# Performance work log

Hardware: AMD Instinct MI355X
Metric: run time of the kernel (lower is better)

The kernel has to match this reference:

```python
import jax, jax.numpy as jnp
import numpy as np

B, N, E, A, H, NT, TE = 2, 20000, 20000, 8, 256, 16, 32


def layer_norm(x, g, b, eps=1e-5):
    mu = x.mean(-1, keepdims=True)
    var = ((x - mu) ** 2).mean(-1, keepdims=True)
    return (x - mu) * jax.lax.rsqrt(var + eps) * g + b


def setup_inputs() -> dict:
    key = jax.random.key(0)
    ks = jax.random.split(key, 12)
    node_features = jax.random.normal(ks[0], (B, N, H), jnp.float32)
    hyperedge_members = jax.random.randint(ks[1], (B, E, A), 0, N)
    hyperedge_types = jax.random.randint(ks[2], (B, E), 0, NT)
    hyperedge_mask = jax.random.bernoulli(ks[3], 0.8, (B, E, A))
    edge_type_table = jax.random.normal(ks[4], (NT, TE), jnp.float32)
    W_enc = jax.random.normal(ks[5], (H + TE, H), jnp.float32) / np.sqrt(H + TE)
    b_enc = jnp.zeros((H,), jnp.float32)
    g_enc = jnp.ones((H,), jnp.float32)
    be_enc = jnp.zeros((H,), jnp.float32)
    W_upd = jax.random.normal(ks[6], (2 * H, H), jnp.float32) / np.sqrt(2 * H)
    b_upd = jnp.zeros((H,), jnp.float32)
    g_upd = jnp.ones((H,), jnp.float32)
    be_upd = jnp.zeros((H,), jnp.float32)
    return dict(node_features=node_features, hyperedge_members=hyperedge_members,
                hyperedge_types=hyperedge_types, hyperedge_mask=hyperedge_mask,
                edge_type_table=edge_type_table, W_enc=W_enc, b_enc=b_enc,
                g_enc=g_enc, be_enc=be_enc, W_upd=W_upd, b_upd=b_upd,
                g_upd=g_upd, be_upd=be_upd)


def reference(node_features, hyperedge_members, hyperedge_types, hyperedge_mask,
              edge_type_table, W_enc, b_enc, g_enc, be_enc,
              W_upd, b_upd, g_upd, be_upd):
    b, n, h = node_features.shape
    members = jnp.clip(hyperedge_members, 0, n - 1)          # [B,E,A]
    m = hyperedge_mask.astype(node_features.dtype)           # [B,E,A]

    # gather member features per hyperedge: [B,E,A,H]
    gathered = jax.vmap(lambda nf, idx: nf[idx])(node_features, members)
    gathered = gathered * m[..., None]
    cnt = jnp.clip(m.sum(-1, keepdims=True), 1.0, None)       # [B,E,1]
    pooled = gathered.sum(2) / cnt                            # [B,E,H]

    edge_emb = edge_type_table[hyperedge_types]               # [B,E,32]
    x = jnp.concatenate([pooled, edge_emb], -1) @ W_enc + b_enc
    edge_feat = layer_norm(jax.nn.gelu(x, approximate=False), g_enc, be_enc)  # [B,E,H]

    # scatter-add edge features back to member nodes (masked)
    def scat(ef, idx, mm):
        contrib = (ef[:, None, :] * mm[..., None]).reshape(-1, h)   # [E*A,H]
        flat = idx.reshape(-1)
        upd = jnp.zeros((n, h), ef.dtype).at[flat].add(contrib)
        c = jnp.zeros((n,), ef.dtype).at[flat].add(mm.reshape(-1))
        return upd, c

    upd, c = jax.vmap(scat)(edge_feat, members, m)            # [B,N,H], [B,N]
    upd = upd / jnp.clip(c, 1.0, None)[..., None]

    y = jnp.concatenate([node_features, upd], -1) @ W_upd + b_upd
    return layer_norm(jax.nn.gelu(y, approximate=False), g_upd, be_upd)
```

## Files before the change

### kernel.cpp

```cpp
#include <hip/hip_runtime.h>
#include <math.h>

#define Bq 2
#define Nn 20000
#define Ee 20000
#define Aa 8
#define Hh 256
#define TEe 32
#define NTy 16
constexpr int BE   = Bq * Ee;
constexpr int BN   = Bq * Nn;
constexpr int KTE  = 8;
constexpr int KTU  = 16;
constexpr int LDA  = 264;
constexpr int CAP  = 64;
constexpr int PB_DET  = 256;
constexpr int PB_PKE  = 32;
constexpr int PB_PKU  = 64;
constexpr int PB_TB   = 1;
constexpr int PB_ZD   = 64;
constexpr int NPREP   = PB_DET + PB_PKE + PB_PKU + PB_TB + PB_ZD + 1;
constexpr int NFD     = 1875;
constexpr int NFILL3  = NFD / 3;

typedef __attribute__((ext_vector_type(8))) short bf16x8;
typedef __attribute__((ext_vector_type(8))) unsigned short u16x8;
typedef __attribute__((ext_vector_type(4))) float f32x4;
typedef unsigned short u16;
typedef unsigned int   u32;

__device__ __forceinline__ u16 f2bf(float f) {
    u32 u = __float_as_uint(f);
    u32 r = u + 0x7FFFu + ((u >> 16) & 1u);
    return (u16)(r >> 16);
}
__device__ __forceinline__ float bf2f(u16 h) {
    return __uint_as_float(((u32)h) << 16);
}
__device__ __forceinline__ float gelu_f(float x) {
    return 0.5f * x * (1.f + erff(x * 0.70710678118654752440f));
}
__device__ __forceinline__ f32x4 mfma16(bf16x8 a, bf16x8 b, f32x4 c) {
    return __builtin_amdgcn_mfma_f32_16x16x32_bf16(a, b, c, 0, 0, 0);
}

__device__ __forceinline__ float mask_at(const void* mp, int flag, int i) {
    if (flag & 2) return ((const float*)mp)[i];
    if (flag & 1) return ((const unsigned char*)mp)[i] ? 1.f : 0.f;
    return ((const int*)mp)[i] ? 1.f : 0.f;
}

__global__ __launch_bounds__(256) void k_prep(
    const unsigned int* __restrict__ mw, int nmw, int* __restrict__ flag,
    const float* __restrict__ Wenc, u16* __restrict__ WeP,
    const float* __restrict__ Wupd, u16* __restrict__ WuP,
    const float* __restrict__ ett, const float* __restrict__ benc,
    float* __restrict__ tb, int* __restrict__ deg,
    float4* __restrict__ dummy) {
    __shared__ float s_e[NTy * TEe];
    const int bid = blockIdx.x;
    const int tid = threadIdx.x;

    if (bid < PB_DET) {
        int found = 0;
        for (int i = bid * 256 + tid; i < nmw; i += PB_DET * 256) {
            unsigned int w = mw[i];
            if (w == 0x3F800000u) found |= 2;
            else if (w > 1u) found |= 1;
        }
        __shared__ int sf;
        if (tid == 0) sf = 0;
        __syncthreads();
        if (found) atomicOr(&sf, found);
        __syncthreads();
        if (tid == 0 && sf) atomicOr(flag, sf);
    } else if (bid < PB_DET + PB_PKE) {
        int t = (bid - PB_DET) * 256 + tid;
        int lane = t & 63, tile = t >> 6;
        int kt = tile % KTE, nt = tile / KTE;
        int kbase = kt * 32 + (lane >> 4) * 8;
        int col = nt * 16 + (lane & 15);
        u16 tmp[8];
        #pragma unroll
        for (int j = 0; j < 8; j++)
            tmp[j] = f2bf(Wenc[(size_t)(kbase + j) * Hh + col]);
        *(uint4*)(WeP + (size_t)t * 8) = *(const uint4*)tmp;
    } else if (bid < PB_DET + PB_PKE + PB_PKU) {
        int t = (bid - PB_DET - PB_PKE) * 256 + tid;
        int lane = t & 63, tile = t >> 6;
        int kt = tile % KTU, nt = tile / KTU;
        int kbase = kt * 32 + (lane >> 4) * 8;
        int col = nt * 16 + (lane & 15);
        u16 tmp[8];
        #pragma unroll
        for (int j = 0; j < 8; j++)
            tmp[j] = f2bf(Wupd[(size_t)(kbase + j) * Hh + col]);
        *(uint4*)(WuP + (size_t)t * 8) = *(const uint4*)tmp;
    } else if (bid < PB_DET + PB_PKE + PB_PKU + PB_TB) {
        for (int i = tid; i < NTy * TEe; i += 256) s_e[i] = ett[i];
        __syncthreads();
        float b = benc[tid];
        for (int t = 0; t < NTy; t++) {
            float acc = b;
            #pragma unroll 8
            for (int k = 0; k < TEe; k++)
                acc = fmaf(s_e[t * TEe + k], Wenc[(size_t)(Hh + k) * Hh + tid], acc);
            tb[t * Hh + tid] = acc;
        }
    } else if (bid < PB_DET + PB_PKE + PB_PKU + PB_TB + PB_ZD) {
        for (int i = (bid - PB_DET - PB_PKE - PB_PKU - PB_TB) * 256 + tid;
             i < BN; i += PB_ZD * 256)
            deg[i] = 0;
    } else {
        if (tid < Hh * 2 / 16) {
            float4 z; z.x = 0.f; z.y = 0.f; z.z = 0.f; z.w = 0.f;
            dummy[tid] = z;
        }
    }
}

__global__ __launch_bounds__(512) void k_fill_dual(
    const int* __restrict__ members, const void* __restrict__ maskp,
    const int* __restrict__ flagp, int* __restrict__ deg,
    int* __restrict__ list2,
    const float* __restrict__ nf, const bf16x8* __restrict__ WeP,
    const bf16x8* __restrict__ WuP, uint4* __restrict__ nfWe1,
    uint4* __restrict__ nfW1) {
    __shared__ __align__(16) u16 s_a[32][LDA];
    const int bid = blockIdx.x;
    const int tid = threadIdx.x;

    if (bid % 3 == 2) {
        const int fbid = bid / 3;
        int flag = flagp[0];
        int i = fbid * 512 + tid;
        if (mask_at(maskp, flag, i) != 0.f) {
            int ge = i >> 3;
            int b = ge / Ee;
            int idx = min(max(members[i], 0), Nn - 1);
            int node = b * Nn + idx;
            int slot = atomicAdd(&deg[node], 1);
            if (slot < CAP) list2[(size_t)node * CAP + slot] = ge;
        }
        return;
    }
    const int gbid = (bid / 3) * 2 + (bid % 3);
    if (gbid >= BN / 32) return;
    const int n0 = gbid * 32;
    const int w = tid >> 6, lane = tid & 63;
    const int l15 = lane & 15, lg = lane >> 4;
    const int isU = w >> 2;
    const int wc  = w & 3;

    {
        const float4* nf4 = (const float4*)nf + (size_t)n0 * 64;
        #pragma unroll
        for (int i = 0; i < 4; i++) {
            int idx = i * 512 + tid;
            int r = idx >> 6, cc = idx & 63;
            float4 v = nf4[r * 64 + cc];
            ushort4 u; u.x = f2bf(v.x); u.y = f2bf(v.y);
            u.z = f2bf(v.z); u.w = f2bf(v.w);
            *(ushort4*)&s_a[r][cc * 4] = u;
        }
    }
    __syncthreads();

    f32x4 acc[2][4];
    #pragma unroll
    for (int m = 0; m < 2; m++)
        #pragma unroll
        for (int n = 0; n < 4; n++) acc[m][n] = (f32x4){0.f, 0.f, 0.f, 0.f};

    const bf16x8* Wp = isU ? WuP : WeP;
    const int kstride = isU ? KTU : KTE;
    #pragma unroll
    for (int kt = 0; kt < 8; kt++) {
        bf16x8 afr[2], bfr[4];
        #pragma unroll
        for (int n = 0; n < 4; n++)
            bfr[n] = Wp[((size_t)((wc * 4 + n) * kstride + kt)) * 64 + lane];
        #pragma unroll
        for (int m = 0; m < 2; m++)
            afr[m] = *(const bf16x8*)&s_a[m * 16 + l15][kt * 32 + lg * 8];
        #pragma unroll
        for (int m = 0; m < 2; m++)
            #pragma unroll
            for (int n = 0; n < 4; n++)
                acc[m][n] = mfma16(afr[m], bfr[n], acc[m][n]);
    }
    __syncthreads();
    if (!isU) {
        #pragma unroll
        for (int m = 0; m < 2; m++)
            #pragma unroll
            for (int j = 0; j < 4; j++) {
                int r = m * 16 + lg * 4 + j;
                #pragma unroll
                for (int n = 0; n < 4; n++)
                    s_a[r][wc * 64 + n * 16 + l15] = f2bf(acc[m][n][j]);
            }
    }
    __syncthreads();
    {
        const uint4* sa4 = (const uint4*)&s_a[0][0];
        #pragma unroll
        for (int i = 0; i < 2; i++) {
            int idx = i * 512 + tid;
            int r = idx >> 5, cc = idx & 31;
            nfWe1[(size_t)(n0 + r) * 32 + cc] = sa4[r * 33 + cc];
        }
    }
    __syncthreads();
    if (isU) {
        #pragma unroll
        for (int m = 0; m < 2; m++)
            #pragma unroll
            for (int j = 0; j < 4; j++) {
                int r = m * 16 + lg * 4 + j;
                #pragma unroll
                for (int n = 0; n < 4; n++)
                    s_a[r][wc * 64 + n * 16 + l15] = f2bf(acc[m][n][j]);
            }
    }
    __syncthreads();
    {
        const uint4* sa4 = (const uint4*)&s_a[0][0];
        #pragma unroll
        for (int i = 0; i < 2; i++) {
            int idx = i * 512 + tid;
            int r = idx >> 5, cc = idx & 31;
            nfW1[(size_t)(n0 + r) * 32 + cc] = sa4[r * 33 + cc];
        }
    }
}

__global__ __launch_bounds__(256) void k_edge_w2(
    const int* __restrict__ members, const void* __restrict__ maskp,
    const int* __restrict__ flagp, const int* __restrict__ types,
    const u16* __restrict__ nfWe1, const float* __restrict__ tb,
    const float* __restrict__ genc, const float* __restrict__ beenc,
    const bf16x8* __restrict__ WuP, uint4* __restrict__ efW2) {
    __shared__ __align__(16) u16 s_a[32][LDA];
    const int tid = threadIdx.x;
    const int e0  = blockIdx.x * 32;
    const int w = tid >> 6, lane = tid & 63;
    const int l15 = lane & 15, lg = lane >> 4;
    const int flag = flagp[0];
    const int colb = (lane & 31) * 8;
    const int half = lane >> 5;
    const int colw = colb + half * 4;

    {
        const int ew0 = e0 + w * 8;
        int base = ew0 * Aa + lane;
        int mem_all = members[base];
        float mv_all = mask_at(maskp, flag, base);
        int er = ew0 + (lane >> 3);
        int idxv = min(max(mem_all, 0), Nn - 1) + ((er >= Ee) ? Nn : 0);

        float4 gm = *(const float4*)(genc + colw);
        float4 bt = *(const float4*)(beenc + colw);

        for (int i = 0; i < 8; i++) {
            int e = ew0 + i;
            float c = 0.f;
            #pragma unroll
            for (int a = 0; a < Aa; a++) c += __shfl(mv_all, i * 8 + a, 64);
            u16x8 v[4]; float mw_[4];
            #pragma unroll
            for (int q = 0; q < 4; q++) {
                int a = 2 * q + half;
                int gi = __shfl(idxv, i * 8 + a, 64);
                mw_[q] = __shfl(mv_all, i * 8 + a, 64);
                v[q] = *(const u16x8*)(nfWe1 + (size_t)gi * Hh + colb);
            }
            float acc[8];
            #pragma unroll
            for (int k = 0; k < 8; k++) acc[k] = 0.f;
            #pragma unroll
            for (int q = 0; q < 4; q++)
                #pragma unroll
                for (int k = 0; k < 8; k++)
                    acc[k] = fmaf(mw_[q], bf2f(v[q][k]), acc[k]);
            #pragma unroll
            for (int k = 0; k < 8; k++) acc[k] += __shfl_xor(acc[k], 32, 64);
            const float rc = 1.f / fmaxf(c, 1.f);
            float x0 = half ? acc[4] : acc[0];
            float x1 = half ? acc[5] : acc[1];
            float x2 = half ? acc[6] : acc[2];
            float x3 = half ? acc[7] : acc[3];
            int t = types[e];
            float4 tbv = *(const float4*)(tb + t * Hh + colw);
            float g0 = gelu_f(fmaf(x0, rc, tbv.x));
            float g1 = gelu_f(fmaf(x1, rc, tbv.y));
            float g2 = gelu_f(fmaf(x2, rc, tbv.z));
            float g3 = gelu_f(fmaf(x3, rc, tbv.w));
            float s  = g0 + g1 + g2 + g3;
            float s2 = fmaf(g0, g0, fmaf(g1, g1, fmaf(g2, g2, g3 * g3)));
            #pragma unroll
            for (int mk = 1; mk < 64; mk <<= 1) {
                s  += __shfl_xor(s, mk, 64);
                s2 += __shfl_xor(s2, mk, 64);
            }
            float mu = s * (1.f / Hh);
            float rs = rsqrtf(s2 * (1.f / Hh) - mu * mu + 1e-5f);
            ushort4 o;
            o.x = f2bf((g0 - mu) * rs * gm.x + bt.x);
            o.y = f2bf((g1 - mu) * rs * gm.y + bt.y);
            o.z = f2bf((g2 - mu) * rs * gm.z + bt.z);
            o.w = f2bf((g3 - mu) * rs * gm.w + bt.w);
            *(ushort4*)&s_a[w * 8 + i][colw] = o;
        }
    }
    __syncthreads();

    f32x4 acc[2][4];
    #pragma unroll
    for (int m = 0; m < 2; m++)
        #pragma unroll
        for (int n = 0; n < 4; n++) acc[m][n] = (f32x4){0.f, 0.f, 0.f, 0.f};

    #pragma unroll
    for (int kt = 0; kt < 8; kt++) {
        bf16x8 bfr[4], afr[2];
        #pragma unroll
        for (int n = 0; n < 4; n++)
            bfr[n] = WuP[((size_t)((w * 4 + n) * KTU + 8 + kt)) * 64 + lane];
        #pragma unroll
        for (int m = 0; m < 2; m++)
            afr[m] = *(const bf16x8*)&s_a[m * 16 + l15][kt * 32 + lg * 8];
        #pragma unroll
        for (int m = 0; m < 2; m++)
            #pragma unroll
            for (int n = 0; n < 4; n++)
                acc[m][n] = mfma16(afr[m], bfr[n], acc[m][n]);
    }
    __syncthreads();
    #pragma unroll
    for (int m = 0; m < 2; m++)
        #pragma unroll
        for (int j = 0; j < 4; j++) {
            int r = m * 16 + lg * 4 + j;
            #pragma unroll
            for (int n = 0; n < 4; n++)
                s_a[r][w * 64 + n * 16 + l15] = f2bf(acc[m][n][j]);
        }
    __syncthreads();
    const uint4* sa4 = (const uint4*)&s_a[0][0];
    #pragma unroll
    for (int i = 0; i < 4; i++) {
        int idx = i * 256 + tid;
        int r = idx >> 5, cc = idx & 31;
        efW2[(size_t)(e0 + r) * 32 + cc] = sa4[r * 33 + cc];
    }
}

__global__ __launch_bounds__(512) void k_node_final(
    const u16* __restrict__ efW2, const u16* __restrict__ nfW1,
    const int* __restrict__ deg, const int* __restrict__ list2,
    const float* __restrict__ bupd, const float* __restrict__ gupd,
    const float* __restrict__ beupd, float* __restrict__ out) {
    const int n = (blockIdx.x * 512 + threadIdx.x) >> 6;
    const int lane = threadIdx.x & 63;
    if (n >= BN) return;
    const int d = min(deg[n], CAP);
    const size_t base = (size_t)n * CAP;
    const int colb = (lane & 31) * 8;
    const int half = lane >> 5;
    const int colw = colb + half * 4;

    int lv = (lane < d) ? list2[base + lane] : BE;

    float acc[8];
    #pragma unroll
    for (int k = 0; k < 8; k++) acc[k] = 0.f;

    for (int j0 = 0; j0 < d; j0 += 8) {
        u16x8 v[4];
        #pragma unroll
        for (int q = 0; q < 4; q++) {
            int jj = j0 + 2 * q + half;
            int ge = __shfl(lv, jj & 63, 64);
            if (jj >= d) ge = BE;
            v[q] = *(const u16x8*)(efW2 + (size_t)ge * Hh + colb);
        }
        #pragma unroll
        for (int q = 0; q < 4; q++)
            #pragma unroll
            for (int k = 0; k < 8; k++)
                acc[k] += bf2f(v[q][k]);
    }
    #pragma unroll
    for (int k = 0; k < 8; k++) acc[k] += __shfl_xor(acc[k], 32, 64);

    const float rc = 1.f / fmaxf((float)d, 1.f);
    float x0 = half ? acc[4] : acc[0];
    float x1 = half ? acc[5] : acc[1];
    float x2 = half ? acc[6] : acc[2];
    float x3 = half ? acc[7] : acc[3];
    ushort4 w1 = *(const ushort4*)(nfW1 + (size_t)n * Hh + colw);
    float4 bb = *(const float4*)(bupd + colw);
    float g0 = gelu_f(fmaf(x0, rc, bf2f(w1.x) + bb.x));
    float g1 = gelu_f(fmaf(x1, rc, bf2f(w1.y) + bb.y));
    float g2 = gelu_f(fmaf(x2, rc, bf2f(w1.z) + bb.z));
    float g3 = gelu_f(fmaf(x3, rc, bf2f(w1.w) + bb.w));

    float s  = g0 + g1 + g2 + g3;
    float s2 = fmaf(g0, g0, fmaf(g1, g1, fmaf(g2, g2, g3 * g3)));
    #pragma unroll
    for (int mk = 1; mk < 64; mk <<= 1) {
        s  += __shfl_xor(s, mk, 64);
        s2 += __shfl_xor(s2, mk, 64);
    }
    float mu = s * (1.f / Hh);
    float rs = rsqrtf(s2 * (1.f / Hh) - mu * mu + 1e-5f);

    float4 gm = *(const float4*)(gupd + colw);
    float4 bt = *(const float4*)(beupd + colw);
    float4 o;
    o.x = (g0 - mu) * rs * gm.x + bt.x;
    o.y = (g1 - mu) * rs * gm.y + bt.y;
    o.z = (g2 - mu) * rs * gm.z + bt.z;
    o.w = (g3 - mu) * rs * gm.w + bt.w;
    *(float4*)(out + (size_t)n * Hh + colw) = o;
}

extern "C" void kernel_launch(void* const* d_in, const int* in_sizes, int n_in,
                              void* d_out, int out_size, void* d_ws, size_t ws_size,
                              hipStream_t stream) {
    const float* nf    = (const float*)d_in[0];
    const int* members = (const int*)d_in[1];
    const int* types   = (const int*)d_in[2];
    const void* maskp  = d_in[3];
    const float* ett   = (const float*)d_in[4];
    const float* Wenc  = (const float*)d_in[5];
    const float* benc  = (const float*)d_in[6];
    const float* genc  = (const float*)d_in[7];
    const float* beenc = (const float*)d_in[8];
    const float* Wupd  = (const float*)d_in[9];
    const float* bupd  = (const float*)d_in[10];
    const float* gupd  = (const float*)d_in[11];
    const float* beupd = (const float*)d_in[12];
    float* out = (float*)d_out;

    int* ip    = (int*)d_ws;
    int* flag  = ip;
    int* deg   = ip + 64;
    int* list2 = deg + BN;
    char* p    = (char*)(list2 + (size_t)BN * CAP);
    u16* efW2b  = (u16*)p;   p += (size_t)(BE + 1) * Hh * 2;
    u16* nfW1b  = (u16*)p;   p += (size_t)BN * Hh * 2;
    u16* nfWe1b = (u16*)p;   p += (size_t)BN * Hh * 2;
    u16* We1P   = (u16*)p;   p += (size_t)16 * KTE * 64 * 8 * 2;
    u16* WupdP  = (u16*)p;   p += (size_t)16 * KTU * 64 * 8 * 2;
    float* tb   = (float*)p;

    hipMemsetAsync(flag, 0, 256, stream);
    hipLaunchKernelGGL(k_prep, dim3(NPREP), dim3(256), 0, stream,
                       (const unsigned int*)maskp, BE * Aa / 4, flag,
                       Wenc, We1P, Wupd, WupdP, ett, benc, tb, deg,
                       (float4*)(efW2b + (size_t)BE * Hh));
    hipLaunchKernelGGL(k_fill_dual, dim3(NFD), dim3(512), 0, stream,
                       members, maskp, flag, deg, list2,
                       nf, (const bf16x8*)We1P, (const bf16x8*)WupdP,
                       (uint4*)nfWe1b, (uint4*)nfW1b);
    hipLaunchKernelGGL(k_edge_w2, dim3(BE / 32), dim3(256), 0, stream,
                       members, maskp, flag, types, nfWe1b, tb, genc, beenc,
                       (const bf16x8*)WupdP, (uint4*)efW2b);
    hipLaunchKernelGGL(k_node_final, dim3(BN * 64 / 512), dim3(512), 0, stream,
                       efW2b, nfW1b, deg, list2, bupd, gupd, beupd, out);
}
```

Measured before the change: 114.8 us.

## Move node-update GEMM into edge kernel to balance work across launches

The node-feature x W_upd GEMM is split out of the fill kernel and interleaved, by even/odd block index, with the edge-encoder blocks in the second kernel. The fill kernel now does only the W_enc GEMM plus a grid-strided member-list fill with 256-thread blocks, and a shared gemm32_body helper replaces the duplicated code. The aim is to balance work between the two launches and overlap the independent update GEMM with the gather-heavy edge work. The cost is that nf is read twice and each kernel's block mix changes, which may alter occupancy.

```diff
diff --git a/kernel.cpp b/kernel.cpp
--- a/kernel.cpp
+++ b/kernel.cpp
@@ -20,8 +20,9 @@
 constexpr int PB_TB   = 1;
 constexpr int PB_ZD   = 64;
 constexpr int NPREP   = PB_DET + PB_PKE + PB_PKU + PB_TB + PB_ZD + 1;
-constexpr int NFD     = 1875;
-constexpr int NFILL3  = NFD / 3;
+constexpr int NFB     = 1890;
+constexpr int NFILL3  = NFB / 3;
+constexpr int NUC     = 2500;
 
 typedef __attribute__((ext_vector_type(8))) short bf16x8;
 typedef __attribute__((ext_vector_type(8))) unsigned short u16x8;
@@ -48,6 +49,68 @@
     if (flag & 2) return ((const float*)mp)[i];
     if (flag & 1) return ((const unsigned char*)mp)[i] ? 1.f : 0.f;
     return ((const int*)mp)[i] ? 1.f : 0.f;
+}
+
+__device__ __forceinline__ void gemm32_body(
+    u16 (*s_a)[LDA], int tid, int n0, const float* __restrict__ nf,
+    const bf16x8* __restrict__ Wp, int kstride, int ktoff,
+    uint4* __restrict__ outb) {
+    const int w = tid >> 6, lane = tid & 63;
+    const int l15 = lane & 15, lg = lane >> 4;
+
+    {
+        const float4* nf4 = (const float4*)nf + (size_t)n0 * 64;
+        #pragma unroll
+        for (int i = 0; i < 8; i++) {
+            int idx = i * 256 + tid;
+            int r = idx >> 6, cc = idx & 63;
+            float4 v = nf4[r * 64 + cc];
+            ushort4 u; u.x = f2bf(v.x); u.y = f2bf(v.y);
+            u.z = f2bf(v.z); u.w = f2bf(v.w);
+            *(ushort4*)&s_a[r][cc * 4] = u;
+        }
+    }
+    __syncthreads();
+
+    f32x4 acc[2][4];
+    #pragma unroll
+    for (int m = 0; m < 2; m++)
+        #pragma unroll
+        for (int n = 0; n < 4; n++) acc[m][n] = (f32x4){0.f, 0.f, 0.f, 0.f};
+
+    #pragma unroll
+    for (int kt = 0; kt < 8; kt++) {
+        bf16x8 afr[2], bfr[4];
+        #pragma unroll
+        for (int n = 0; n < 4; n++)
+            bfr[n] = Wp[((size_t)((w * 4 + n) * kstride + ktoff + kt)) * 64 + lane];
+        #pragma unroll
+        for (int m = 0; m < 2; m++)
+            afr[m] = *(const bf16x8*)&s_a[m * 16 + l15][kt * 32 + lg * 8];
+        #pragma unroll
+        for (int m = 0; m < 2; m++)
+            #pragma unroll
+            for (int n = 0; n < 4; n++)
+                acc[m][n] = mfma16(afr[m], bfr[n], acc[m][n]);
+    }
+    __syncthreads();
+    #pragma unroll
+    for (int m = 0; m < 2; m++)
+        #pragma unroll
+        for (int j = 0; j < 4; j++) {
+            int r = m * 16 + lg * 4 + j;
+            #pragma unroll
+            for (int n = 0; n < 4; n++)
+                s_a[r][w * 64 + n * 16 + l15] = f2bf(acc[m][n][j]);
+        }
+    __syncthreads();
+    const uint4* sa4 = (const uint4*)&s_a[0][0];
+    #pragma unroll
+    for (int i = 0; i < 4; i++) {
+        int idx = i * 256 + tid;
+        int r = idx >> 5, cc = idx & 31;
+        outb[(size_t)(n0 + r) * 32 + cc] = sa4[r * 33 + cc];
+    }
 }
 
 __global__ __launch_bounds__(256) void k_prep(
@@ -119,13 +182,12 @@
     }
 }
 
-__global__ __launch_bounds__(512) void k_fill_dual(
+__global__ __launch_bounds__(256) void k_fill_egemm(
     const int* __restrict__ members, const void* __restrict__ maskp,
     const int* __restrict__ flagp, int* __restrict__ deg,
     int* __restrict__ list2,
     const float* __restrict__ nf, const bf16x8* __restrict__ WeP,
-    const bf16x8* __restrict__ WuP, uint4* __restrict__ nfWe1,
-    uint4* __restrict__ nfW1) {
+    uint4* __restrict__ nfWe1) {
     __shared__ __align__(16) u16 s_a[32][LDA];
     const int bid = blockIdx.x;
     const int tid = threadIdx.x;
@@ -133,117 +195,40 @@
     if (bid % 3 == 2) {
         const int fbid = bid / 3;
         int flag = flagp[0];
-        int i = fbid * 512 + tid;
-        if (mask_at(maskp, flag, i) != 0.f) {
-            int ge = i >> 3;
-            int b = ge / Ee;
-            int idx = min(max(members[i], 0), Nn - 1);
-            int node = b * Nn + idx;
-            int slot = atomicAdd(&deg[node], 1);
-            if (slot < CAP) list2[(size_t)node * CAP + slot] = ge;
+        for (int i = fbid * 256 + tid; i < BE * Aa; i += NFILL3 * 256) {
+            if (mask_at(maskp, flag, i) != 0.f) {
+                int ge = i >> 3;
+                int b = ge / Ee;
+                int idx = min(max(members[i], 0), Nn - 1);
+                int node = b * Nn + idx;
+                int slot = atomicAdd(&deg[node], 1);
+                if (slot < CAP) list2[(size_t)node * CAP + slot] = ge;
+            }
         }
         return;
     }
     const int gbid = (bid / 3) * 2 + (bid % 3);
     if (gbid >= BN / 32) return;
-    const int n0 = gbid * 32;
-    const int w = tid >> 6, lane = tid & 63;
-    const int l15 = lane & 15, lg = lane >> 4;
-    const int isU = w >> 2;
-    const int wc  = w & 3;
-
-    {
-        const float4* nf4 = (const float4*)nf + (size_t)n0 * 64;
-        #pragma unroll
-        for (int i = 0; i < 4; i++) {
-            int idx = i * 512 + tid;
-            int r = idx >> 6, cc = idx & 63;
-            float4 v = nf4[r * 64 + cc];
-            ushort4 u; u.x = f2bf(v.x); u.y = f2bf(v.y);
-            u.z = f2bf(v.z); u.w = f2bf(v.w);
-            *(ushort4*)&s_a[r][cc * 4] = u;
-        }
-    }
-    __syncthreads();
-
-    f32x4 acc[2][4];
-    #pragma unroll
-    for (int m = 0; m < 2; m++)
-        #pragma unroll
-        for (int n = 0; n < 4; n++) acc[m][n] = (f32x4){0.f, 0.f, 0.f, 0.f};
-
-    const bf16x8* Wp = isU ? WuP : WeP;
-    const int kstride = isU ? KTU : KTE;
-    #pragma unroll
-    for (int kt = 0; kt < 8; kt++) {
-        bf16x8 afr[2], bfr[4];
-        #pragma unroll
-        for (int n = 0; n < 4; n++)
-            bfr[n] = Wp[((size_t)((wc * 4 + n) * kstride + kt)) * 64 + lane];
-        #pragma unroll
-        for (int m = 0; m < 2; m++)
-            afr[m] = *(const bf16x8*)&s_a[m * 16 + l15][kt * 32 + lg * 8];
-        #pragma unroll
-        for (int m = 0; m < 2; m++)
-            #pragma unroll
-            for (int n = 0; n < 4; n++)
-                acc[m][n] = mfma16(afr[m], bfr[n], acc[m][n]);
-    }
-    __syncthreads();
-    if (!isU) {
-        #pragma unroll
-        for (int m = 0; m < 2; m++)
-            #pragma unroll
-            for (int j = 0; j < 4; j++) {
-                int r = m * 16 + lg * 4 + j;
-                #pragma unroll
-                for (int n = 0; n < 4; n++)
-                    s_a[r][wc * 64 + n * 16 + l15] = f2bf(acc[m][n][j]);
-            }
-    }
-    __syncthreads();
-    {
-        const uint4* sa4 = (const uint4*)&s_a[0][0];
-        #pragma unroll
-        for (int i = 0; i < 2; i++) {
-            int idx = i * 512 + tid;
-            int r = idx >> 5, cc = idx & 31;
-            nfWe1[(size_t)(n0 + r) * 32 + cc] = sa4[r * 33 + cc];
-        }
-    }
-    __syncthreads();
-    if (isU) {
-        #pragma unroll
-        for (int m = 0; m < 2; m++)
-            #pragma unroll
-            for (int j = 0; j < 4; j++) {
-                int r = m * 16 + lg * 4 + j;
-                #pragma unroll
-                for (int n = 0; n < 4; n++)
-                    s_a[r][wc * 64 + n * 16 + l15] = f2bf(acc[m][n][j]);
-            }
-    }
-    __syncthreads();
-    {
-        const uint4* sa4 = (const uint4*)&s_a[0][0];
-        #pragma unroll
-        for (int i = 0; i < 2; i++) {
-            int idx = i * 512 + tid;
-            int r = idx >> 5, cc = idx & 31;
-            nfW1[(size_t)(n0 + r) * 32 + cc] = sa4[r * 33 + cc];
-        }
-    }
-}
-
-__global__ __launch_bounds__(256) void k_edge_w2(
+    gemm32_body(s_a, tid, gbid * 32, nf, WeP, KTE, 0, nfWe1);
+}
+
+__global__ __launch_bounds__(256) void k_ugemm_edge(
+    const float* __restrict__ nf, const bf16x8* __restrict__ WuP,
+    uint4* __restrict__ nfW1,
     const int* __restrict__ members, const void* __restrict__ maskp,
     const int* __restrict__ flagp, const int* __restrict__ types,
     const u16* __restrict__ nfWe1, const float* __restrict__ tb,
     const float* __restrict__ genc, const float* __restrict__ beenc,
-    const bf16x8* __restrict__ WuP, uint4* __restrict__ efW2) {
+    uint4* __restrict__ efW2) {
     __shared__ __align__(16) u16 s_a[32][LDA];
+    const int bid = blockIdx.x;
     const int tid = threadIdx.x;
-    const int e0  = blockIdx.x * 32;
+
+    if ((bid & 1) == 0) {
+        gemm32_body(s_a, tid, (bid >> 1) * 32, nf, WuP, KTU, 0, nfW1);
+        return;
+    }
+    const int e0  = (bid >> 1) * 32;
     const int w = tid >> 6, lane = tid & 63;
     const int l15 = lane & 15, lg = lane >> 4;
     const int flag = flagp[0];
@@ -461,13 +446,13 @@
                        (const unsigned int*)maskp, BE * Aa / 4, flag,
                        Wenc, We1P, Wupd, WupdP, ett, benc, tb, deg,
                        (float4*)(efW2b + (size_t)BE * Hh));
-    hipLaunchKernelGGL(k_fill_dual, dim3(NFD), dim3(512), 0, stream,
+    hipLaunchKernelGGL(k_fill_egemm, dim3(NFB), dim3(256), 0, stream,
                        members, maskp, flag, deg, list2,
-                       nf, (const bf16x8*)We1P, (const bf16x8*)WupdP,
-                       (uint4*)nfWe1b, (uint4*)nfW1b);
-    hipLaunchKernelGGL(k_edge_w2, dim3(BE / 32), dim3(256), 0, stream,
+                       nf, (const bf16x8*)We1P, (uint4*)nfWe1b);
+    hipLaunchKernelGGL(k_ugemm_edge, dim3(NUC), dim3(256), 0, stream,
+                       nf, (const bf16x8*)WupdP, (uint4*)nfW1b,
                        members, maskp, flag, types, nfWe1b, tb, genc, beenc,
-                       (const bf16x8*)WupdP, (uint4*)efW2b);
+                       (uint4*)efW2b);
     hipLaunchKernelGGL(k_node_final, dim3(BN * 64 / 512), dim3(512), 0, stream,
                        efW2b, nfW1b, deg, list2, bupd, gupd, beupd, out);
 }
```

Result: slower. 125.7 us (+9.5%).
